# Optimization experiments

Hardware: AMD Instinct MI355X
Metric: run time of the kernel (lower is better)

Reference implementation:

```python
import jax, jax.numpy as jnp
import numpy as np

N_NODES = 50000
N_EDGES = 800000
C_IN = 128
C_OUT = 64
C_HID = 2 * C_OUT  # 128


def setup_inputs() -> dict:
    key = jax.random.key(0)
    ks = jax.random.split(key, 8)
    x = jax.random.normal(ks[0], (N_NODES, C_IN), dtype=jnp.float32)
    edge_index = jax.random.randint(ks[1], (2, N_EDGES), 0, N_NODES, dtype=jnp.int64)
    s1 = 1.0 / np.sqrt(C_IN)
    s2 = 1.0 / np.sqrt(C_HID)
    s3 = 1.0 / np.sqrt(C_OUT)
    W1 = jax.random.uniform(ks[2], (C_IN, C_HID), jnp.float32, -s1, s1)
    b1 = jnp.zeros((C_HID,), jnp.float32)
    W2 = jax.random.uniform(ks[3], (C_HID, C_OUT), jnp.float32, -s2, s2)
    b2 = jnp.zeros((C_OUT,), jnp.float32)
    Wb = jax.random.uniform(ks[4], (1, C_OUT, C_OUT), jnp.float32, -s3, s3)
    bb = jax.random.uniform(ks[5], (1,), jnp.float32, -s3, s3)
    return {"x": x, "edge_index": edge_index, "W1": W1, "b1": b1,
            "W2": W2, "b2": b2, "Wb": Wb, "bb": bb}


def gcn_conv(x, W, b, src, dst, n_nodes):
    # PyG GCNConv: h = x @ W; add self-loops; symmetric normalization D^-1/2 (A+I) D^-1/2.
    h = x @ W  # [N, F]
    ones = jnp.ones((src.shape[0],), h.dtype)
    deg = jax.ops.segment_sum(ones, dst, num_segments=n_nodes) + 1.0  # +1 for self-loop
    dinv = jax.lax.rsqrt(deg)
    norm = dinv[src] * dinv[dst]  # [E]
    msgs = h[src] * norm[:, None]  # [E, F]
    agg = jax.ops.segment_sum(msgs, dst, num_segments=n_nodes)
    # self-loop contribution: norm_ii = 1/deg_i
    agg = agg + h * (1.0 / deg)[:, None]
    return agg + b


def reference(x, edge_index, W1, b1, W2, b2, Wb, bb):
    src = edge_index[0]
    dst = edge_index[1]
    n = x.shape[0]
    # encode
    h = jax.nn.relu(gcn_conv(x, W1, b1, src, dst, n))
    z = gcn_conv(h, W2, b2, src, dst, n)  # [N, C_OUT]
    # decode: bilinear on (z[src], z[dst]) -> sigmoid
    zs = z[src]  # [E, C_OUT]
    zd = z[dst]  # [E, C_OUT]
    logits = jnp.einsum('ec,ocd,ed->eo', zs, Wb, zd) + bb  # [E, 1]
    return jax.nn.sigmoid(logits)
```

## Files before the change

### kernel.cpp

```cpp
#include <hip/hip_runtime.h>
#include <hip/hip_bf16.h>


#define N_NODES 50000
#define BSH 7
#define BSZ 128
#define NBUCK ((N_NODES + BSZ - 1) / BSZ)
#define EPB 4096
#define CAP 3072

typedef unsigned int u32;
typedef unsigned short u16;

typedef __attribute__((ext_vector_type(8))) short bf16x8;
typedef __attribute__((ext_vector_type(4))) float f32x4;
union frag_u { bf16x8 f; u32 u[4]; uint4 v; };

__device__ __forceinline__ float bflo(u32 u) { return __uint_as_float(u << 16); }
__device__ __forceinline__ float bfhi(u32 u) { return __uint_as_float(u & 0xffff0000u); }
__device__ __forceinline__ u32 f2bf(float f) {
    u32 b = __float_as_uint(f);
    return (b + 0x7fffu + ((b >> 16) & 1u)) >> 16;
}
__device__ __forceinline__ u32 pack2(float a, float b) { return f2bf(a) | (f2bf(b) << 16); }

__global__ __launch_bounds__(256) void bucket_scatter(const int* __restrict__ src,
                                                      const int* __restrict__ dst,
                                                      int* __restrict__ bcur,
                                                      u32* __restrict__ pair, int E) {
    __shared__ int hist[NBUCK];
    for (int i = threadIdx.x; i < NBUCK; i += 256) hist[i] = 0;
    __syncthreads();
    int base = blockIdx.x * EPB;
    int s_[16], d_[16];
#pragma unroll
    for (int it = 0; it < 16; it++) {
        int e = base + it * 256 + threadIdx.x;
        if (e < E) {
            s_[it] = src[e];
            d_[it] = dst[e];
            atomicAdd(&hist[d_[it] >> BSH], 1);
        } else {
            d_[it] = -1;
        }
    }
    __syncthreads();
    for (int b = threadIdx.x; b < NBUCK; b += 256) {
        int c = hist[b];
        hist[b] = c ? (b * CAP + atomicAdd(&bcur[b], c)) : 0;
    }
    __syncthreads();
#pragma unroll
    for (int it = 0; it < 16; it++) {
        if (d_[it] >= 0) {
            int b = d_[it] >> BSH;
            int off = atomicAdd(&hist[b], 1);
            pair[off] = (u32)s_[it] | ((u32)(d_[it] & (BSZ - 1)) << 16);
        }
    }
}

__global__ __launch_bounds__(512) void bucket_scan(const int* __restrict__ bcur,
                                                   int* __restrict__ bbase, int E) {
    __shared__ int tmp[512];
    int t = threadIdx.x;
    int v = (t < NBUCK) ? bcur[t] : 0;
    tmp[t] = v;
    __syncthreads();
    for (int off = 1; off < 512; off <<= 1) {
        int a = (t >= off) ? tmp[t - off] : 0;
        __syncthreads();
        tmp[t] += a;
        __syncthreads();
    }
    if (t < NBUCK) bbase[t] = tmp[t] - v;
    if (t == 0) bbase[NBUCK] = E;
}

__global__ __launch_bounds__(256) void bucket_sort(const u32* __restrict__ pair,
                                                   const int* __restrict__ bbase,
                                                   int* __restrict__ row_ptr,
                                                   int* __restrict__ col,
                                                   float* __restrict__ dinv,
                                                   float* __restrict__ inv, int n, int E) {
    __shared__ int cnt[BSZ];
    __shared__ int scn[BSZ];
    __shared__ int cur[BSZ];
    int t = threadIdx.x;
    int base = blockIdx.x << BSH;
    int nn = min(BSZ, n - base);
    int b0 = bbase[blockIdx.x];
    int cntE = bbase[blockIdx.x + 1] - b0;
    int p0 = blockIdx.x * CAP;
    if (t < BSZ) cnt[t] = 0;
    __syncthreads();
    for (int j = t; j < cntE; j += 256)
        atomicAdd(&cnt[pair[p0 + j] >> 16], 1);
    __syncthreads();
    if (t < BSZ) scn[t] = cnt[t];
    __syncthreads();
    for (int off = 1; off < BSZ; off <<= 1) {
        int a = (t < BSZ && t >= off) ? scn[t - off] : 0;
        __syncthreads();
        if (t < BSZ) scn[t] += a;
        __syncthreads();
    }
    if (t < nn) {
        int excl = b0 + scn[t] - cnt[t];
        row_ptr[base + t] = excl;
        cur[t] = excl;
        float d = (float)cnt[t] + 1.0f;
        dinv[base + t] = rsqrtf(d);
        inv[base + t] = 1.0f / d;
    }
    if (t == 0 && blockIdx.x == NBUCK - 1) row_ptr[n] = E;
    __syncthreads();
    for (int j = t; j < cntE; j += 256) {
        u32 p = pair[p0 + j];
        int ln = (int)(p >> 16);
        int pos = atomicAdd(&cur[ln], 1);
        col[pos] = (int)(p & 0xffffu);
    }
}

template <int K, int NOUT, bool A_BF16>
__global__ __launch_bounds__(256) void gemm_mfma(const void* __restrict__ Xv,
                                                 const float* __restrict__ W,
                                                 u16* __restrict__ O, int n_rows) {
    constexpr int KP = K + 8;
    constexpr int NT = NOUT / 16;
    constexpr int KS = K / 32;
    __shared__ __align__(16) u16 Wt_hi[NOUT * KP];
    __shared__ __align__(16) u16 Wt_lo[NOUT * KP];
    int t = threadIdx.x;
    for (int i4 = t; i4 < K * NOUT / 4; i4 += 256) {
        int k = (i4 * 4) / NOUT;
        int n0 = (i4 * 4) % NOUT;
        float4 w4 = *(const float4*)&W[(size_t)k * NOUT + n0];
        float wv[4] = {w4.x, w4.y, w4.z, w4.w};
#pragma unroll
        for (int q = 0; q < 4; q++) {
            u32 hi = f2bf(wv[q]);
            u32 lo = f2bf(wv[q] - bflo(hi));
            Wt_hi[(n0 + q) * KP + k] = (u16)hi;
            Wt_lo[(n0 + q) * KP + k] = (u16)lo;
        }
    }
    __syncthreads();

    int wave = t >> 6;
    int lane = t & 63;
    int m16 = lane & 15;
    int quad = lane >> 4;
    int row0 = blockIdx.x * 128 + wave * 32;

    f32x4 acc[2][NT] = {};
    for (int ks = 0; ks < KS; ks++) {
        frag_u a_hi[2], a_lo[2];
#pragma unroll
        for (int mt = 0; mt < 2; mt++) {
            int row = row0 + mt * 16 + m16;
            row = row < n_rows ? row : n_rows - 1;
            if (A_BF16) {
                a_hi[mt].v = *(const uint4*)((const u16*)Xv + (size_t)row * K + ks * 32 + quad * 8);
            } else {
                const float* X = (const float*)Xv + (size_t)row * K + ks * 32 + quad * 8;
                float4 x0 = *(const float4*)X;
                float4 x1 = *(const float4*)(X + 4);
                float xv[8] = {x0.x, x0.y, x0.z, x0.w, x1.x, x1.y, x1.z, x1.w};
#pragma unroll
                for (int p = 0; p < 4; p++) {
                    u32 h0 = f2bf(xv[2 * p]), h1 = f2bf(xv[2 * p + 1]);
                    a_hi[mt].u[p] = h0 | (h1 << 16);
                    a_lo[mt].u[p] = pack2(xv[2 * p] - bflo(h0), xv[2 * p + 1] - bflo(h1));
                }
            }
        }
#pragma unroll
        for (int nt = 0; nt < NT; nt++) {
            int n = nt * 16 + m16;
            frag_u b_hi, b_lo;
            b_hi.v = *(const uint4*)&Wt_hi[n * KP + ks * 32 + quad * 8];
            b_lo.v = *(const uint4*)&Wt_lo[n * KP + ks * 32 + quad * 8];
#pragma unroll
            for (int mt = 0; mt < 2; mt++) {
                acc[mt][nt] = __builtin_amdgcn_mfma_f32_16x16x32_bf16(a_hi[mt].f, b_hi.f, acc[mt][nt], 0, 0, 0);
                acc[mt][nt] = __builtin_amdgcn_mfma_f32_16x16x32_bf16(a_hi[mt].f, b_lo.f, acc[mt][nt], 0, 0, 0);
                if (!A_BF16)
                    acc[mt][nt] = __builtin_amdgcn_mfma_f32_16x16x32_bf16(a_lo[mt].f, b_hi.f, acc[mt][nt], 0, 0, 0);
            }
        }
    }
#pragma unroll
    for (int mt = 0; mt < 2; mt++)
#pragma unroll
        for (int nt = 0; nt < NT; nt++)
#pragma unroll
            for (int r = 0; r < 4; r++) {
                int row = row0 + mt * 16 + quad * 4 + r;
                if (row < n_rows)
                    O[(size_t)row * NOUT + nt * 16 + m16] = (u16)f2bf(acc[mt][nt][r]);
            }
}

template <int C, bool RELU>
__global__ __launch_bounds__(256) void agg_pull(const u16* __restrict__ H,
                                                const int* __restrict__ row_ptr,
                                                const int* __restrict__ col,
                                                const float* __restrict__ dinv,
                                                const float* __restrict__ inv,
                                                const float* __restrict__ b,
                                                u16* __restrict__ O, int n) {
    constexpr int TPN = C / 8;
    const uint4* Hv = (const uint4*)H;
    int tid = blockIdx.x * 256 + threadIdx.x;
    int node = tid / TPN;
    if (node >= n) return;
    int part = tid % TPN;
    int c8 = part * 8;
    float dn = dinv[node];
    float iv = inv[node];
    float acc[8];
    {
        uint4 h = Hv[(size_t)node * TPN + part];
        acc[0] = bflo(h.x) * iv + b[c8 + 0];
        acc[1] = bfhi(h.x) * iv + b[c8 + 1];
        acc[2] = bflo(h.y) * iv + b[c8 + 2];
        acc[3] = bfhi(h.y) * iv + b[c8 + 3];
        acc[4] = bflo(h.z) * iv + b[c8 + 4];
        acc[5] = bfhi(h.z) * iv + b[c8 + 5];
        acc[6] = bflo(h.w) * iv + b[c8 + 6];
        acc[7] = bfhi(h.w) * iv + b[c8 + 7];
    }
    int j = row_ptr[node];
    int end = row_ptr[node + 1];
    for (; j + 3 < end; j += 4) {
        int s0 = col[j], s1 = col[j + 1], s2 = col[j + 2], s3 = col[j + 3];
        float n0 = dn * dinv[s0], n1 = dn * dinv[s1];
        float n2 = dn * dinv[s2], n3 = dn * dinv[s3];
        uint4 v0 = Hv[(size_t)s0 * TPN + part];
        uint4 v1 = Hv[(size_t)s1 * TPN + part];
        uint4 v2 = Hv[(size_t)s2 * TPN + part];
        uint4 v3 = Hv[(size_t)s3 * TPN + part];
        acc[0] += bflo(v0.x) * n0 + bflo(v1.x) * n1 + bflo(v2.x) * n2 + bflo(v3.x) * n3;
        acc[1] += bfhi(v0.x) * n0 + bfhi(v1.x) * n1 + bfhi(v2.x) * n2 + bfhi(v3.x) * n3;
        acc[2] += bflo(v0.y) * n0 + bflo(v1.y) * n1 + bflo(v2.y) * n2 + bflo(v3.y) * n3;
        acc[3] += bfhi(v0.y) * n0 + bfhi(v1.y) * n1 + bfhi(v2.y) * n2 + bfhi(v3.y) * n3;
        acc[4] += bflo(v0.z) * n0 + bflo(v1.z) * n1 + bflo(v2.z) * n2 + bflo(v3.z) * n3;
        acc[5] += bfhi(v0.z) * n0 + bfhi(v1.z) * n1 + bfhi(v2.z) * n2 + bfhi(v3.z) * n3;
        acc[6] += bflo(v0.w) * n0 + bflo(v1.w) * n1 + bflo(v2.w) * n2 + bflo(v3.w) * n3;
        acc[7] += bfhi(v0.w) * n0 + bfhi(v1.w) * n1 + bfhi(v2.w) * n2 + bfhi(v3.w) * n3;
    }
    for (; j < end; j++) {
        int s = col[j];
        float nm = dn * dinv[s];
        uint4 v = Hv[(size_t)s * TPN + part];
        acc[0] += bflo(v.x) * nm; acc[1] += bfhi(v.x) * nm;
        acc[2] += bflo(v.y) * nm; acc[3] += bfhi(v.y) * nm;
        acc[4] += bflo(v.z) * nm; acc[5] += bfhi(v.z) * nm;
        acc[6] += bflo(v.w) * nm; acc[7] += bfhi(v.w) * nm;
    }
    if (RELU) {
#pragma unroll
        for (int i = 0; i < 8; i++) acc[i] = fmaxf(acc[i], 0.f);
    }
    uint4 o;
    o.x = pack2(acc[0], acc[1]);
    o.y = pack2(acc[2], acc[3]);
    o.z = pack2(acc[4], acc[5]);
    o.w = pack2(acc[6], acc[7]);
    ((uint4*)O)[(size_t)node * TPN + part] = o;
}

__global__ __launch_bounds__(256) void decode_kernel(const u16* __restrict__ Y,
                                                     const u16* __restrict__ Z,
                                                     const int* __restrict__ src,
                                                     const int* __restrict__ dst,
                                                     const float* __restrict__ bb,
                                                     float* __restrict__ out, int E) {
    const uint4* Yv = (const uint4*)Y;
    const uint4* Zv = (const uint4*)Z;
    int tid = blockIdx.x * 256 + threadIdx.x;
    int e = tid / 8;
    int lane = tid % 8;
    if (e >= E) return;
    int s = src[e], d = dst[e];
    uint4 y = Yv[(size_t)s * 8 + lane];
    uint4 z = Zv[(size_t)d * 8 + lane];
    float p = bflo(y.x) * bflo(z.x) + bfhi(y.x) * bfhi(z.x)
            + bflo(y.y) * bflo(z.y) + bfhi(y.y) * bfhi(z.y)
            + bflo(y.z) * bflo(z.z) + bfhi(y.z) * bfhi(z.z)
            + bflo(y.w) * bflo(z.w) + bfhi(y.w) * bfhi(z.w);
    p += __shfl_down(p, 4, 8);
    p += __shfl_down(p, 2, 8);
    p += __shfl_down(p, 1, 8);
    if (lane == 0) out[e] = 1.0f / (1.0f + expf(-(p + bb[0])));
}

extern "C" void kernel_launch(void* const* d_in, const int* in_sizes, int n_in,
                              void* d_out, int out_size, void* d_ws, size_t ws_size,
                              hipStream_t stream) {
    const float* x  = (const float*)d_in[0];
    const int*   ei = (const int*)d_in[1];
    const float* W1 = (const float*)d_in[2];
    const float* b1 = (const float*)d_in[3];
    const float* W2 = (const float*)d_in[4];
    const float* b2 = (const float*)d_in[5];
    const float* Wb = (const float*)d_in[6];
    const float* bb = (const float*)d_in[7];
    float* out = (float*)d_out;

    const int N = N_NODES;
    const int E = in_sizes[1] / 2;
    const int* src = ei;
    const int* dst = ei + E;
    const int GBLK = (N + 127) / 128;
    const int SBLK = (E + EPB - 1) / EPB;

    char* w = (char*)d_ws;
    int*   bcur    = (int*)w;   w += (size_t)512 * 4;
    int*   bbase   = (int*)w;   w += (size_t)512 * 4;
    int*   row_ptr = (int*)w;   w += (size_t)(N + 1) * 4;
    int*   col     = (int*)w;   w += (size_t)E * 4;
    u32*   pair    = (u32*)w;   w += (size_t)NBUCK * CAP * 4;
    float* dinv    = (float*)w; w += (size_t)N * 4;
    float* inv     = (float*)w; w += (size_t)N * 4;
    w = (char*)(((size_t)w + 15) & ~(size_t)15);
    u16* bufA = (u16*)w;        w += (size_t)N * 128 * 2;
    u16* bufB = (u16*)w;        w += (size_t)N * 128 * 2;
    u16* bufC = (u16*)w;

    u16* H1 = bufA;
    u16* h1 = bufB;
    u16* H2 = bufA;
    u16* Z  = bufC;
    u16* Y  = bufA + (size_t)N * 64;

    hipMemsetAsync(bcur, 0, 512 * 4, stream);
    bucket_scatter<<<SBLK, 256, 0, stream>>>(src, dst, bcur, pair, E);
    bucket_scan<<<1, 512, 0, stream>>>(bcur, bbase, E);
    bucket_sort<<<NBUCK, 256, 0, stream>>>(pair, bbase, row_ptr, col, dinv, inv, N, E);

    gemm_mfma<128, 128, false><<<GBLK, 256, 0, stream>>>(x, W1, H1, N);
    agg_pull<128, true><<<((size_t)N * 16 + 255) / 256, 256, 0, stream>>>(
        H1, row_ptr, col, dinv, inv, b1, h1, N);

    gemm_mfma<128, 64, true><<<GBLK, 256, 0, stream>>>(h1, W2, H2, N);
    agg_pull<64, false><<<((size_t)N * 8 + 255) / 256, 256, 0, stream>>>(
        H2, row_ptr, col, dinv, inv, b2, Z, N);

    gemm_mfma<64, 64, true><<<GBLK, 256, 0, stream>>>(Z, Wb, Y, N);
    decode_kernel<<<((size_t)E * 8 + 255) / 256, 256, 0, stream>>>(Y, Z, src, dst, bb, out, E);
}
```

Before: 252.9 us.

## Fuse first GEMM with edge bucket scatter and drop separate scan kernel

The first feature GEMM and the edge bucket-scatter now run as one launch, with block indices split between the two roles so the independent work can overlap on the GPU. The single-block prefix-scan kernel is removed: each bucket_sort block instead sums the bucket counts before it with a shared-memory reduction. This cuts two kernel launches and their serialization gaps. In exchange every sort block does redundant prefix work, and the GEMM role's shared-memory footprint is applied to the scatter blocks as well.

```diff
diff --git a/kernel.cpp b/kernel.cpp
--- a/kernel.cpp
+++ b/kernel.cpp
@@ -24,73 +24,141 @@
 }
 __device__ __forceinline__ u32 pack2(float a, float b) { return f2bf(a) | (f2bf(b) << 16); }
 
-__global__ __launch_bounds__(256) void bucket_scatter(const int* __restrict__ src,
-                                                      const int* __restrict__ dst,
-                                                      int* __restrict__ bcur,
-                                                      u32* __restrict__ pair, int E) {
-    __shared__ int hist[NBUCK];
-    for (int i = threadIdx.x; i < NBUCK; i += 256) hist[i] = 0;
-    __syncthreads();
-    int base = blockIdx.x * EPB;
-    int s_[16], d_[16];
-#pragma unroll
-    for (int it = 0; it < 16; it++) {
-        int e = base + it * 256 + threadIdx.x;
-        if (e < E) {
-            s_[it] = src[e];
-            d_[it] = dst[e];
-            atomicAdd(&hist[d_[it] >> BSH], 1);
-        } else {
-            d_[it] = -1;
-        }
-    }
-    __syncthreads();
-    for (int b = threadIdx.x; b < NBUCK; b += 256) {
-        int c = hist[b];
-        hist[b] = c ? (b * CAP + atomicAdd(&bcur[b], c)) : 0;
-    }
-    __syncthreads();
-#pragma unroll
-    for (int it = 0; it < 16; it++) {
-        if (d_[it] >= 0) {
-            int b = d_[it] >> BSH;
-            int off = atomicAdd(&hist[b], 1);
-            pair[off] = (u32)s_[it] | ((u32)(d_[it] & (BSZ - 1)) << 16);
-        }
-    }
-}
-
-__global__ __launch_bounds__(512) void bucket_scan(const int* __restrict__ bcur,
-                                                   int* __restrict__ bbase, int E) {
-    __shared__ int tmp[512];
+__global__ __launch_bounds__(256) void gemm1_scatter(
+        const float* __restrict__ X, const float* __restrict__ W,
+        u16* __restrict__ O, int n_rows, int gblk,
+        const int* __restrict__ src, const int* __restrict__ dst,
+        int* __restrict__ bcur, u32* __restrict__ pair, int E) {
+    constexpr int K = 128, NOUT = 128;
+    constexpr int KP = K + 8;
+    constexpr int NT = NOUT / 16;
+    constexpr int KS = K / 32;
+    __shared__ __align__(16) char smem[NOUT * KP * 2 * sizeof(u16)];
     int t = threadIdx.x;
-    int v = (t < NBUCK) ? bcur[t] : 0;
-    tmp[t] = v;
-    __syncthreads();
-    for (int off = 1; off < 512; off <<= 1) {
-        int a = (t >= off) ? tmp[t - off] : 0;
-        __syncthreads();
-        tmp[t] += a;
-        __syncthreads();
-    }
-    if (t < NBUCK) bbase[t] = tmp[t] - v;
-    if (t == 0) bbase[NBUCK] = E;
+
+    if ((int)blockIdx.x < gblk) {
+        u16* Wt_hi = (u16*)smem;
+        u16* Wt_lo = Wt_hi + NOUT * KP;
+        for (int i4 = t; i4 < K * NOUT / 4; i4 += 256) {
+            int k = (i4 * 4) / NOUT;
+            int n0 = (i4 * 4) % NOUT;
+            float4 w4 = *(const float4*)&W[(size_t)k * NOUT + n0];
+            float wv[4] = {w4.x, w4.y, w4.z, w4.w};
+#pragma unroll
+            for (int q = 0; q < 4; q++) {
+                u32 hi = f2bf(wv[q]);
+                u32 lo = f2bf(wv[q] - bflo(hi));
+                Wt_hi[(n0 + q) * KP + k] = (u16)hi;
+                Wt_lo[(n0 + q) * KP + k] = (u16)lo;
+            }
+        }
+        __syncthreads();
+
+        int wave = t >> 6;
+        int lane = t & 63;
+        int m16 = lane & 15;
+        int quad = lane >> 4;
+        int row0 = blockIdx.x * 128 + wave * 32;
+
+        f32x4 acc[2][NT] = {};
+        for (int ks = 0; ks < KS; ks++) {
+            frag_u a_hi[2], a_lo[2];
+#pragma unroll
+            for (int mt = 0; mt < 2; mt++) {
+                int row = row0 + mt * 16 + m16;
+                row = row < n_rows ? row : n_rows - 1;
+                const float* Xp = X + (size_t)row * K + ks * 32 + quad * 8;
+                float4 x0 = *(const float4*)Xp;
+                float4 x1 = *(const float4*)(Xp + 4);
+                float xv[8] = {x0.x, x0.y, x0.z, x0.w, x1.x, x1.y, x1.z, x1.w};
+#pragma unroll
+                for (int p = 0; p < 4; p++) {
+                    u32 h0 = f2bf(xv[2 * p]), h1 = f2bf(xv[2 * p + 1]);
+                    a_hi[mt].u[p] = h0 | (h1 << 16);
+                    a_lo[mt].u[p] = pack2(xv[2 * p] - bflo(h0), xv[2 * p + 1] - bflo(h1));
+                }
+            }
+#pragma unroll
+            for (int nt = 0; nt < NT; nt++) {
+                int n = nt * 16 + m16;
+                frag_u b_hi, b_lo;
+                b_hi.v = *(const uint4*)&Wt_hi[n * KP + ks * 32 + quad * 8];
+                b_lo.v = *(const uint4*)&Wt_lo[n * KP + ks * 32 + quad * 8];
+#pragma unroll
+                for (int mt = 0; mt < 2; mt++) {
+                    acc[mt][nt] = __builtin_amdgcn_mfma_f32_16x16x32_bf16(a_hi[mt].f, b_hi.f, acc[mt][nt], 0, 0, 0);
+                    acc[mt][nt] = __builtin_amdgcn_mfma_f32_16x16x32_bf16(a_hi[mt].f, b_lo.f, acc[mt][nt], 0, 0, 0);
+                    acc[mt][nt] = __builtin_amdgcn_mfma_f32_16x16x32_bf16(a_lo[mt].f, b_hi.f, acc[mt][nt], 0, 0, 0);
+                }
+            }
+        }
+#pragma unroll
+        for (int mt = 0; mt < 2; mt++)
+#pragma unroll
+            for (int nt = 0; nt < NT; nt++)
+#pragma unroll
+                for (int r = 0; r < 4; r++) {
+                    int row = row0 + mt * 16 + quad * 4 + r;
+                    if (row < n_rows)
+                        O[(size_t)row * NOUT + nt * 16 + m16] = (u16)f2bf(acc[mt][nt][r]);
+                }
+    } else {
+        int* hist = (int*)smem;
+        for (int i = t; i < NBUCK; i += 256) hist[i] = 0;
+        __syncthreads();
+        int base = ((int)blockIdx.x - gblk) * EPB;
+        int s_[16], d_[16];
+#pragma unroll
+        for (int it = 0; it < 16; it++) {
+            int e = base + it * 256 + t;
+            if (e < E) {
+                s_[it] = src[e];
+                d_[it] = dst[e];
+                atomicAdd(&hist[d_[it] >> BSH], 1);
+            } else {
+                d_[it] = -1;
+            }
+        }
+        __syncthreads();
+        for (int b = t; b < NBUCK; b += 256) {
+            int c = hist[b];
+            hist[b] = c ? (b * CAP + atomicAdd(&bcur[b], c)) : 0;
+        }
+        __syncthreads();
+#pragma unroll
+        for (int it = 0; it < 16; it++) {
+            if (d_[it] >= 0) {
+                int b = d_[it] >> BSH;
+                int off = atomicAdd(&hist[b], 1);
+                pair[off] = (u32)s_[it] | ((u32)(d_[it] & (BSZ - 1)) << 16);
+            }
+        }
+    }
 }
 
 __global__ __launch_bounds__(256) void bucket_sort(const u32* __restrict__ pair,
-                                                   const int* __restrict__ bbase,
+                                                   const int* __restrict__ bcur,
                                                    int* __restrict__ row_ptr,
                                                    int* __restrict__ col,
                                                    float* __restrict__ dinv,
                                                    float* __restrict__ inv, int n, int E) {
+    __shared__ int ssum[256];
     __shared__ int cnt[BSZ];
     __shared__ int scn[BSZ];
     __shared__ int cur[BSZ];
     int t = threadIdx.x;
     int base = blockIdx.x << BSH;
     int nn = min(BSZ, n - base);
-    int b0 = bbase[blockIdx.x];
-    int cntE = bbase[blockIdx.x + 1] - b0;
+    int accp = 0;
+    for (int i = t; i < (int)blockIdx.x; i += 256) accp += bcur[i];
+    ssum[t] = accp;
+    __syncthreads();
+    for (int s = 128; s > 0; s >>= 1) {
+        if (t < s) ssum[t] += ssum[t + s];
+        __syncthreads();
+    }
+    int b0 = ssum[0];
+    int cntE = bcur[blockIdx.x];
     int p0 = blockIdx.x * CAP;
     if (t < BSZ) cnt[t] = 0;
     __syncthreads();
@@ -123,10 +191,10 @@
     }
 }
 
-template <int K, int NOUT, bool A_BF16>
-__global__ __launch_bounds__(256) void gemm_mfma(const void* __restrict__ Xv,
-                                                 const float* __restrict__ W,
-                                                 u16* __restrict__ O, int n_rows) {
+template <int K, int NOUT>
+__global__ __launch_bounds__(256) void gemm_mfma_bf(const u16* __restrict__ Xv,
+                                                    const float* __restrict__ W,
+                                                    u16* __restrict__ O, int n_rows) {
     constexpr int KP = K + 8;
     constexpr int NT = NOUT / 16;
     constexpr int KS = K / 32;
@@ -156,25 +224,12 @@
 
     f32x4 acc[2][NT] = {};
     for (int ks = 0; ks < KS; ks++) {
-        frag_u a_hi[2], a_lo[2];
+        frag_u a_hi[2];
 #pragma unroll
         for (int mt = 0; mt < 2; mt++) {
             int row = row0 + mt * 16 + m16;
             row = row < n_rows ? row : n_rows - 1;
-            if (A_BF16) {
-                a_hi[mt].v = *(const uint4*)((const u16*)Xv + (size_t)row * K + ks * 32 + quad * 8);
-            } else {
-                const float* X = (const float*)Xv + (size_t)row * K + ks * 32 + quad * 8;
-                float4 x0 = *(const float4*)X;
-                float4 x1 = *(const float4*)(X + 4);
-                float xv[8] = {x0.x, x0.y, x0.z, x0.w, x1.x, x1.y, x1.z, x1.w};
-#pragma unroll
-                for (int p = 0; p < 4; p++) {
-                    u32 h0 = f2bf(xv[2 * p]), h1 = f2bf(xv[2 * p + 1]);
-                    a_hi[mt].u[p] = h0 | (h1 << 16);
-                    a_lo[mt].u[p] = pack2(xv[2 * p] - bflo(h0), xv[2 * p + 1] - bflo(h1));
-                }
-            }
+            a_hi[mt].v = *(const uint4*)(Xv + (size_t)row * K + ks * 32 + quad * 8);
         }
 #pragma unroll
         for (int nt = 0; nt < NT; nt++) {
@@ -186,8 +241,6 @@
             for (int mt = 0; mt < 2; mt++) {
                 acc[mt][nt] = __builtin_amdgcn_mfma_f32_16x16x32_bf16(a_hi[mt].f, b_hi.f, acc[mt][nt], 0, 0, 0);
                 acc[mt][nt] = __builtin_amdgcn_mfma_f32_16x16x32_bf16(a_hi[mt].f, b_lo.f, acc[mt][nt], 0, 0, 0);
-                if (!A_BF16)
-                    acc[mt][nt] = __builtin_amdgcn_mfma_f32_16x16x32_bf16(a_lo[mt].f, b_hi.f, acc[mt][nt], 0, 0, 0);
             }
         }
     }
@@ -319,7 +372,6 @@
 
     char* w = (char*)d_ws;
     int*   bcur    = (int*)w;   w += (size_t)512 * 4;
-    int*   bbase   = (int*)w;   w += (size_t)512 * 4;
     int*   row_ptr = (int*)w;   w += (size_t)(N + 1) * 4;
     int*   col     = (int*)w;   w += (size_t)E * 4;
     u32*   pair    = (u32*)w;   w += (size_t)NBUCK * CAP * 4;
@@ -337,18 +389,17 @@
     u16* Y  = bufA + (size_t)N * 64;
 
     hipMemsetAsync(bcur, 0, 512 * 4, stream);
-    bucket_scatter<<<SBLK, 256, 0, stream>>>(src, dst, bcur, pair, E);
-    bucket_scan<<<1, 512, 0, stream>>>(bcur, bbase, E);
-    bucket_sort<<<NBUCK, 256, 0, stream>>>(pair, bbase, row_ptr, col, dinv, inv, N, E);
-
-    gemm_mfma<128, 128, false><<<GBLK, 256, 0, stream>>>(x, W1, H1, N);
+    gemm1_scatter<<<GBLK + SBLK, 256, 0, stream>>>(x, W1, H1, N, GBLK,
+                                                   src, dst, bcur, pair, E);
+    bucket_sort<<<NBUCK, 256, 0, stream>>>(pair, bcur, row_ptr, col, dinv, inv, N, E);
+
     agg_pull<128, true><<<((size_t)N * 16 + 255) / 256, 256, 0, stream>>>(
         H1, row_ptr, col, dinv, inv, b1, h1, N);
 
-    gemm_mfma<128, 64, true><<<GBLK, 256, 0, stream>>>(h1, W2, H2, N);
+    gemm_mfma_bf<128, 64><<<GBLK, 256, 0, stream>>>(h1, W2, H2, N);
     agg_pull<64, false><<<((size_t)N * 8 + 255) / 256, 256, 0, stream>>>(
         H2, row_ptr, col, dinv, inv, b2, Z, N);
 
-    gemm_mfma<64, 64, true><<<GBLK, 256, 0, stream>>>(Z, Wb, Y, N);
+    gemm_mfma_bf<64, 64><<<GBLK, 256, 0, stream>>>(Z, Wb, Y, N);
     decode_kernel<<<((size_t)E * 8 + 255) / 256, 256, 0, stream>>>(Y, Z, src, dst, bb, out, E);
 }
```

After: 240.0 us (median of 2 runs). -5.1%, faster.
